# Optimization experiments

Hardware: AMD Instinct MI355X
Metric: run time of the kernel (lower is better)

## Reference

```python
import jax, jax.numpy as jnp
import numpy as np

N, S, E, H = 4, 2048, 1024, 16
D = E // H  # head dim = 64


def setup_inputs() -> dict:
    key = jax.random.key(0)
    ks = jax.random.split(key, 8)
    return {
        "values": jax.random.normal(ks[0], (N, S, E), dtype=jnp.float32),
        "keys": jax.random.normal(ks[1], (N, S, E), dtype=jnp.float32),
        "queries": jax.random.normal(ks[2], (N, S, E), dtype=jnp.float32),
        "mask": jnp.ones((N, 1, 1, S), dtype=jnp.int32),
        "Wv": jax.random.normal(ks[3], (D, D), dtype=jnp.float32) / np.sqrt(D),
        "Wk": jax.random.normal(ks[4], (D, D), dtype=jnp.float32) / np.sqrt(D),
        "Wq": jax.random.normal(ks[5], (D, D), dtype=jnp.float32) / np.sqrt(D),
        "W_out": jax.random.normal(ks[6], (E, E), dtype=jnp.float32) / np.sqrt(E),
        "b_out": jnp.zeros((E,), dtype=jnp.float32),
    }


def reference(values, keys, queries, mask, Wv, Wk, Wq, W_out, b_out):
    n, q_len = queries.shape[0], queries.shape[1]
    v = values.reshape(n, -1, H, D)
    k = keys.reshape(n, -1, H, D)
    q = queries.reshape(n, q_len, H, D)
    # per-head linear projections (torch Linear: x @ W.T), shared across heads
    v = jnp.einsum('nlhd,ed->nlhe', v, Wv)
    k = jnp.einsum('nlhd,ed->nlhe', k, Wk)
    q = jnp.einsum('nqhd,ed->nqhe', q, Wq)
    # full score tensor [n, h, q, k], faithful to the original einsum
    energy = jnp.einsum('nqhd,nkhd->nhqk', q, k)
    energy = jnp.where(mask == 0, jnp.float32(-1e20), energy)
    # NOTE: original scales by sqrt(embed_size), not sqrt(head_dim)
    attention = jax.nn.softmax(energy / jnp.sqrt(jnp.float32(E)), axis=3)
    out = jnp.einsum('nhql,nlhd->nqhd', attention, v).reshape(n, q_len, E)
    out = out @ W_out.T + b_out
    return out
```

## Files before the change

kernel.cpp:

```cpp
#include <hip/hip_runtime.h>
#include <stdint.h>

#define N_B 4
#define SEQ 2048
#define EMB 1024
#define NH  16
#define HD  64
#define NHT 64
#define BQ  128
#define BK  64

typedef __attribute__((ext_vector_type(8))) short bf16x8;
typedef __attribute__((ext_vector_type(4))) short bf16x4;
typedef __attribute__((ext_vector_type(4))) float f32x4;

__device__ __forceinline__ short f2bf(float x) {
  unsigned u = __float_as_uint(x);
  u += 0x7fffu + ((u >> 16) & 1u);
  return (short)(u >> 16);
}

__device__ __forceinline__ void glds16(const short* g, short* l) {
  __builtin_amdgcn_global_load_lds(
      (const __attribute__((address_space(1))) unsigned int*)g,
      (__attribute__((address_space(3))) unsigned int*)l, 16, 0, 0);
}

__device__ __forceinline__ int swz_src(int lane) {
  return (((lane & 7) ^ ((lane >> 3) & 7)) * 8) + ((lane >> 3) * 64);
}
__device__ __forceinline__ int swz_rd(int r, int k) {
  return r * 64 + ((k ^ (r & 7)) * 8);
}

__global__ __launch_bounds__(256) void cvt_kernel(const float* __restrict__ W,
                                                  short* __restrict__ Wb) {
  int idx = (blockIdx.x * 256 + threadIdx.x) * 4;
  f32x4 v = *(const f32x4*)(W + idx);
  bf16x4 p;
  p.x = f2bf(v.x); p.y = f2bf(v.y); p.z = f2bf(v.z); p.w = f2bf(v.w);
  *(bf16x4*)(Wb + idx) = p;
}

__global__ __launch_bounds__(256) void projm_kernel(const float* __restrict__ X,
                                                    const float* __restrict__ W,
                                                    short* __restrict__ out,
                                                    int transposed) {
  __shared__ __attribute__((aligned(16))) short Xs[128 * 64];
  __shared__ __attribute__((aligned(16))) short Ws[64 * 64];
  int tid = threadIdx.x;
  int w = tid >> 6, lane = tid & 63;
  int quad = lane >> 4, l15 = lane & 15;
  int sb = blockIdx.x * 128;
  int nh = blockIdx.y;
  int n = nh >> 4, h = nh & 15;
  int r4 = tid >> 2, c0 = (tid & 3) * 16;
  int ch0 = c0 >> 3;
#pragma unroll
  for (int rr = 0; rr < 2; rr++) {
    int row = rr * 64 + r4;
    const float* gp = X + ((size_t)(n * SEQ + sb + row)) * EMB + h * HD + c0;
    f32x4 a = *(const f32x4*)gp, b = *(const f32x4*)(gp + 4);
    f32x4 c = *(const f32x4*)(gp + 8), d = *(const f32x4*)(gp + 12);
    bf16x8 p0, p1;
    p0[0]=f2bf(a.x); p0[1]=f2bf(a.y); p0[2]=f2bf(a.z); p0[3]=f2bf(a.w);
    p0[4]=f2bf(b.x); p0[5]=f2bf(b.y); p0[6]=f2bf(b.z); p0[7]=f2bf(b.w);
    p1[0]=f2bf(c.x); p1[1]=f2bf(c.y); p1[2]=f2bf(c.z); p1[3]=f2bf(c.w);
    p1[4]=f2bf(d.x); p1[5]=f2bf(d.y); p1[6]=f2bf(d.z); p1[7]=f2bf(d.w);
    *(bf16x8*)&Xs[row * 64 + ((ch0 ^ (row & 7)) * 8)] = p0;
    *(bf16x8*)&Xs[row * 64 + (((ch0 + 1) ^ (row & 7)) * 8)] = p1;
  }
  {
    int e = r4;
    const float* wp = W + e * HD + c0;
    f32x4 a = *(const f32x4*)wp, b = *(const f32x4*)(wp + 4);
    f32x4 c = *(const f32x4*)(wp + 8), d = *(const f32x4*)(wp + 12);
    bf16x8 p0, p1;
    p0[0]=f2bf(a.x); p0[1]=f2bf(a.y); p0[2]=f2bf(a.z); p0[3]=f2bf(a.w);
    p0[4]=f2bf(b.x); p0[5]=f2bf(b.y); p0[6]=f2bf(b.z); p0[7]=f2bf(b.w);
    p1[0]=f2bf(c.x); p1[1]=f2bf(c.y); p1[2]=f2bf(c.z); p1[3]=f2bf(c.w);
    p1[4]=f2bf(d.x); p1[5]=f2bf(d.y); p1[6]=f2bf(d.z); p1[7]=f2bf(d.w);
    *(bf16x8*)&Ws[e * 64 + ((ch0 ^ (e & 7)) * 8)] = p0;
    *(bf16x8*)&Ws[e * 64 + (((ch0 + 1) ^ (e & 7)) * 8)] = p1;
  }
  __syncthreads();
  f32x4 acc[2][4] = {};
#pragma unroll
  for (int ch = 0; ch < 2; ch++) {
    bf16x8 af[2], bfr[4];
#pragma unroll
    for (int mi = 0; mi < 2; mi++)
      af[mi] = *(const bf16x8*)&Xs[swz_rd(w * 32 + mi * 16 + l15, ch * 4 + quad)];
#pragma unroll
    for (int ni = 0; ni < 4; ni++)
      bfr[ni] = *(const bf16x8*)&Ws[swz_rd(ni * 16 + l15, ch * 4 + quad)];
#pragma unroll
    for (int mi = 0; mi < 2; mi++)
#pragma unroll
      for (int ni = 0; ni < 4; ni++)
        acc[mi][ni] = __builtin_amdgcn_mfma_f32_16x16x32_bf16(af[mi], bfr[ni], acc[mi][ni], 0, 0, 0);
  }
  if (!transposed) {
#pragma unroll
    for (int mi = 0; mi < 2; mi++)
#pragma unroll
      for (int ni = 0; ni < 4; ni++)
#pragma unroll
        for (int r = 0; r < 4; r++) {
          int s = sb + w * 32 + mi * 16 + quad * 4 + r;
          out[((size_t)nh * SEQ + s) * HD + ni * 16 + l15] = f2bf(acc[mi][ni][r]);
        }
  } else {
#pragma unroll
    for (int mi = 0; mi < 2; mi++)
#pragma unroll
      for (int ni = 0; ni < 4; ni++) {
        int e2 = ni * 16 + l15;
        int s0 = sb + w * 32 + mi * 16 + quad * 4;
        bf16x4 pk;
        pk.x = f2bf(acc[mi][ni][0]); pk.y = f2bf(acc[mi][ni][1]);
        pk.z = f2bf(acc[mi][ni][2]); pk.w = f2bf(acc[mi][ni][3]);
        *(bf16x4*)(out + ((size_t)nh * HD + e2) * SEQ + s0) = pk;
      }
  }
}

__global__ __launch_bounds__(256, 3) void attn_kernel(
    const short* __restrict__ Qp, const short* __restrict__ Kp,
    const short* __restrict__ Vp, const int* __restrict__ maskp,
    short* __restrict__ AO) {
  __shared__ __attribute__((aligned(16))) short Ks[64 * 64];
  __shared__ __attribute__((aligned(16))) short Vts[64 * 64];
  __shared__ __attribute__((aligned(16))) short Qs[128 * 64];
  __shared__ __attribute__((aligned(16))) short Ps[4][32 * 72];
  __shared__ int maskS[64];

  int tid = threadIdx.x;
  int w = tid >> 6, lane = tid & 63;
  int quad = lane >> 4, l15 = lane & 15;
  int nh = blockIdx.x;
  int qt0 = blockIdx.y * BQ;
  int n = nh >> 4, h = nh & 15;
  const float csc = 0.04508422f;
  int ssrc = swz_src(lane);

  const short* qbase = Qp + ((size_t)nh * SEQ + qt0) * HD;
#pragma unroll
  for (int i = 0; i < 4; i++) {
    int idx = (w * 4 + i) * 512;
    glds16(qbase + idx + ssrc, &Qs[idx]);
  }
  __syncthreads();
  bf16x8 qf[2][2];
#pragma unroll
  for (int nt = 0; nt < 2; nt++)
#pragma unroll
    for (int ch = 0; ch < 2; ch++)
      qf[nt][ch] = *(const bf16x8*)&Qs[swz_rd(w * 32 + nt * 16 + l15, ch * 4 + quad)];

  f32x4 Oacc[2][4] = {};
  float lsum[2] = {0.f, 0.f};

  for (int kt = 0; kt < SEQ / BK; kt++) {
    int k0 = kt * BK;
    __syncthreads();
    const short* kb = Kp + ((size_t)nh * SEQ + k0) * HD;
#pragma unroll
    for (int i = 0; i < 2; i++) {
      int idx = (w * 2 + i) * 512;
      glds16(kb + idx + ssrc, &Ks[idx]);
    }
#pragma unroll
    for (int i = 0; i < 2; i++) {
      int ii = w * 2 + i;
      int d = ii * 8 + (lane >> 3);
      const short* vb = Vp + ((size_t)nh * HD + d) * SEQ + k0 +
                        (((lane & 7) ^ ((lane >> 3) & 7)) * 8);
      glds16(vb, &Vts[ii * 512]);
    }
    if (tid < 64) maskS[tid] = maskp[n * SEQ + k0 + tid];
    __syncthreads();

    unsigned long long mb = __ballot(maskS[lane] != 0);

    f32x4 st[4][2];
#pragma unroll
    for (int mt = 0; mt < 4; mt++) {
      bf16x8 kf0 = *(const bf16x8*)&Ks[swz_rd(mt * 16 + l15, quad)];
      bf16x8 kf1 = *(const bf16x8*)&Ks[swz_rd(mt * 16 + l15, 4 + quad)];
#pragma unroll
      for (int nt = 0; nt < 2; nt++) {
        f32x4 a = {0.f, 0.f, 0.f, 0.f};
        a = __builtin_amdgcn_mfma_f32_16x16x32_bf16(kf0, qf[nt][0], a, 0, 0, 0);
        a = __builtin_amdgcn_mfma_f32_16x16x32_bf16(kf1, qf[nt][1], a, 0, 0, 0);
        st[mt][nt] = a;
      }
    }
    if (mb != ~0ull) {
#pragma unroll
      for (int mt = 0; mt < 4; mt++)
#pragma unroll
        for (int r = 0; r < 4; r++) {
          int kk = mt * 16 + quad * 4 + r;
          if (!((mb >> kk) & 1)) { st[mt][0][r] = -1e20f; st[mt][1][r] = -1e20f; }
        }
    }
#pragma unroll
    for (int nt = 0; nt < 2; nt++)
#pragma unroll
      for (int mt = 0; mt < 4; mt++)
#pragma unroll
        for (int r = 0; r < 4; r++) {
          float p = __builtin_amdgcn_exp2f(st[mt][nt][r] * csc);
          st[mt][nt][r] = p;
          lsum[nt] += p;
        }
    short* psw = &Ps[w][0];
#pragma unroll
    for (int nt = 0; nt < 2; nt++)
#pragma unroll
      for (int mt = 0; mt < 4; mt++) {
        bf16x4 pk;
        pk.x = f2bf(st[mt][nt][0]); pk.y = f2bf(st[mt][nt][1]);
        pk.z = f2bf(st[mt][nt][2]); pk.w = f2bf(st[mt][nt][3]);
        *(bf16x4*)&psw[(nt * 16 + l15) * 72 + mt * 16 + quad * 4] = pk;
      }
    __builtin_amdgcn_wave_barrier();

#pragma unroll
    for (int ch = 0; ch < 2; ch++) {
      bf16x8 pf[2];
#pragma unroll
      for (int qt = 0; qt < 2; qt++)
        pf[qt] = *(const bf16x8*)&psw[(qt * 16 + l15) * 72 + ch * 32 + quad * 8];
#pragma unroll
      for (int dt = 0; dt < 4; dt++) {
        bf16x8 vf = *(const bf16x8*)&Vts[swz_rd(dt * 16 + l15, ch * 4 + quad)];
#pragma unroll
        for (int qt = 0; qt < 2; qt++)
          Oacc[qt][dt] = __builtin_amdgcn_mfma_f32_16x16x32_bf16(pf[qt], vf, Oacc[qt][dt], 0, 0, 0);
      }
    }
  }
#pragma unroll
  for (int nt = 0; nt < 2; nt++) {
    lsum[nt] += __shfl_xor(lsum[nt], 16);
    lsum[nt] += __shfl_xor(lsum[nt], 32);
  }
#pragma unroll
  for (int qt = 0; qt < 2; qt++)
#pragma unroll
    for (int r = 0; r < 4; r++) {
      float lr = __shfl(lsum[qt], quad * 4 + r);
      float inv = 1.0f / lr;
      int qrow = qt0 + w * 32 + qt * 16 + quad * 4 + r;
      size_t rowb = ((size_t)n * SEQ + qrow) * EMB + h * HD;
#pragma unroll
      for (int dt = 0; dt < 4; dt++)
        AO[rowb + dt * 16 + l15] = f2bf(Oacc[qt][dt][r] * inv);
    }
}

__global__ __launch_bounds__(256, 3) void gemm_kernel(const short* __restrict__ A,
                                                      const short* __restrict__ B,
                                                      const float* __restrict__ bias,
                                                      float* __restrict__ C) {
  __shared__ __attribute__((aligned(16))) short As[128 * 64];
  __shared__ __attribute__((aligned(16))) short Bs[128 * 64];
  int tid = threadIdx.x;
  int w = tid >> 6, lane = tid & 63;
  int quad = lane >> 4, l15 = lane & 15;
  int m0 = blockIdx.x * 128, n0 = blockIdx.y * 128;
  int mw = (w & 1) * 64, nw = (w >> 1) * 64;
  int lrow = lane >> 3;
  int lcg = ((lane & 7) ^ ((lane >> 3) & 7)) * 8;
  f32x4 acc[4][4] = {};
  for (int kt = 0; kt < 16; kt++) {
    int k0 = kt * 64;
    __syncthreads();
#pragma unroll
    for (int i = 0; i < 4; i++) {
      int ii = w * 4 + i;
      int r = ii * 8 + lrow;
      glds16(A + (size_t)(m0 + r) * 1024 + k0 + lcg, &As[ii * 512]);
      glds16(B + (size_t)(n0 + r) * 1024 + k0 + lcg, &Bs[ii * 512]);
    }
    __syncthreads();
#pragma unroll
    for (int ch = 0; ch < 2; ch++) {
      bf16x8 af[4], bfr[4];
#pragma unroll
      for (int mi = 0; mi < 4; mi++)
        af[mi] = *(const bf16x8*)&As[swz_rd(mw + mi * 16 + l15, ch * 4 + quad)];
#pragma unroll
      for (int ni = 0; ni < 4; ni++)
        bfr[ni] = *(const bf16x8*)&Bs[swz_rd(nw + ni * 16 + l15, ch * 4 + quad)];
#pragma unroll
      for (int mi = 0; mi < 4; mi++)
#pragma unroll
        for (int ni = 0; ni < 4; ni++)
          acc[mi][ni] = __builtin_amdgcn_mfma_f32_16x16x32_bf16(af[mi], bfr[ni], acc[mi][ni], 0, 0, 0);
    }
  }
#pragma unroll
  for (int ni = 0; ni < 4; ni++) {
    int col = n0 + nw + ni * 16 + l15;
    float bv = bias[col];
#pragma unroll
    for (int mi = 0; mi < 4; mi++) {
      int rb = m0 + mw + mi * 16 + quad * 4;
#pragma unroll
      for (int r = 0; r < 4; r++)
        C[(size_t)(rb + r) * 1024 + col] = acc[mi][ni][r] + bv;
    }
  }
}

extern "C" void kernel_launch(void* const* d_in, const int* in_sizes, int n_in,
                              void* d_out, int out_size, void* d_ws, size_t ws_size,
                              hipStream_t stream) {
  const float* values  = (const float*)d_in[0];
  const float* keys    = (const float*)d_in[1];
  const float* queries = (const float*)d_in[2];
  const int*   mask    = (const int*)d_in[3];
  const float* Wv = (const float*)d_in[4];
  const float* Wk = (const float*)d_in[5];
  const float* Wq = (const float*)d_in[6];
  const float* Wo = (const float*)d_in[7];
  const float* bo = (const float*)d_in[8];
  float* out = (float*)d_out;

  short* ws = (short*)d_ws;
  short* Qp = ws;
  short* Kp = Qp + (size_t)NHT * SEQ * HD;
  short* Vp = Kp + (size_t)NHT * SEQ * HD;
  short* AO = Vp + (size_t)NHT * SEQ * HD;
  short* Wb = AO + (size_t)N_B * SEQ * EMB;

  cvt_kernel<<<dim3(1024), dim3(256), 0, stream>>>(Wo, Wb);
  dim3 pg(SEQ / 128, NHT);
  projm_kernel<<<pg, dim3(256), 0, stream>>>(queries, Wq, Qp, 0);
  projm_kernel<<<pg, dim3(256), 0, stream>>>(keys, Wk, Kp, 0);
  projm_kernel<<<pg, dim3(256), 0, stream>>>(values, Wv, Vp, 1);
  dim3 ag(NHT, SEQ / BQ);
  attn_kernel<<<ag, dim3(256), 0, stream>>>(Qp, Kp, Vp, mask, AO);
  dim3 gg(8192 / 128, 1024 / 128);
  gemm_kernel<<<gg, dim3(256), 0, stream>>>(AO, Wb, bo, out);
}
```

Baseline: 303.9 us.

## Double-buffer attention and GEMM loads, merge projection launches, use packed bf16 converts

Folds the weight-conversion kernel and the three projection launches into one launch, using grid z to pick Q, K, V or the W_out conversion. The attention kernel now double-buffers K/V/mask tiles in LDS so the next tile's load overlaps current compute, with one barrier per iteration. Its P scratch reuses the Q buffer with an XOR swizzle instead of padding, which lowers LDS use. The output GEMM is double-buffered too, with launch bounds lowered to 2 blocks per CU because it now needs twice the LDS. Float-to-bf16 rounding uses the hardware packed-convert builtin when it is available.

```diff
diff --git a/kernel.cpp b/kernel.cpp
--- a/kernel.cpp
+++ b/kernel.cpp
@@ -20,6 +20,18 @@
   return (short)(u >> 16);
 }
 
+#if __has_builtin(__builtin_amdgcn_cvt_pk_bf16_f32)
+typedef __attribute__((ext_vector_type(2))) __bf16 bf16v2;
+__device__ __forceinline__ unsigned pkbf(float a, float b) {
+  bf16v2 r = __builtin_amdgcn_cvt_pk_bf16_f32(a, b);
+  union { bf16v2 v; unsigned u; } c; c.v = r; return c.u;
+}
+#else
+__device__ __forceinline__ unsigned pkbf(float a, float b) {
+  return (unsigned)(unsigned short)f2bf(a) | ((unsigned)(unsigned short)f2bf(b) << 16);
+}
+#endif
+
 __device__ __forceinline__ void glds16(const short* g, short* l) {
   __builtin_amdgcn_global_load_lds(
       (const __attribute__((address_space(1))) unsigned int*)g,
@@ -33,22 +45,28 @@
   return r * 64 + ((k ^ (r & 7)) * 8);
 }
 
-__global__ __launch_bounds__(256) void cvt_kernel(const float* __restrict__ W,
-                                                  short* __restrict__ Wb) {
-  int idx = (blockIdx.x * 256 + threadIdx.x) * 4;
-  f32x4 v = *(const f32x4*)(W + idx);
-  bf16x4 p;
-  p.x = f2bf(v.x); p.y = f2bf(v.y); p.z = f2bf(v.z); p.w = f2bf(v.w);
-  *(bf16x4*)(Wb + idx) = p;
-}
-
-__global__ __launch_bounds__(256) void projm_kernel(const float* __restrict__ X,
-                                                    const float* __restrict__ W,
-                                                    short* __restrict__ out,
-                                                    int transposed) {
+__global__ __launch_bounds__(256) void projm_kernel(
+    const float* __restrict__ Xq, const float* __restrict__ Xk, const float* __restrict__ Xv,
+    const float* __restrict__ Wq, const float* __restrict__ Wk, const float* __restrict__ Wv,
+    short* __restrict__ Qp, short* __restrict__ Kp, short* __restrict__ Vp,
+    const float* __restrict__ Wo, short* __restrict__ Wb) {
+  int tid = threadIdx.x;
+  int z = blockIdx.z;
+  if (z == 3) {
+    int flat = blockIdx.x + blockIdx.y * 16;
+    int idx = (flat * 256 + tid) * 4;
+    f32x4 v = *(const f32x4*)(Wo + idx);
+    uint2 u; u.x = pkbf(v.x, v.y); u.y = pkbf(v.z, v.w);
+    *(uint2*)(Wb + idx) = u;
+    return;
+  }
+  const float* X = (z == 0) ? Xq : (z == 1) ? Xk : Xv;
+  const float* W = (z == 0) ? Wq : (z == 1) ? Wk : Wv;
+  short* out = (z == 0) ? Qp : (z == 1) ? Kp : Vp;
+  int transposed = (z == 2);
+
   __shared__ __attribute__((aligned(16))) short Xs[128 * 64];
   __shared__ __attribute__((aligned(16))) short Ws[64 * 64];
-  int tid = threadIdx.x;
   int w = tid >> 6, lane = tid & 63;
   int quad = lane >> 4, l15 = lane & 15;
   int sb = blockIdx.x * 128;
@@ -62,26 +80,26 @@
     const float* gp = X + ((size_t)(n * SEQ + sb + row)) * EMB + h * HD + c0;
     f32x4 a = *(const f32x4*)gp, b = *(const f32x4*)(gp + 4);
     f32x4 c = *(const f32x4*)(gp + 8), d = *(const f32x4*)(gp + 12);
-    bf16x8 p0, p1;
-    p0[0]=f2bf(a.x); p0[1]=f2bf(a.y); p0[2]=f2bf(a.z); p0[3]=f2bf(a.w);
-    p0[4]=f2bf(b.x); p0[5]=f2bf(b.y); p0[6]=f2bf(b.z); p0[7]=f2bf(b.w);
-    p1[0]=f2bf(c.x); p1[1]=f2bf(c.y); p1[2]=f2bf(c.z); p1[3]=f2bf(c.w);
-    p1[4]=f2bf(d.x); p1[5]=f2bf(d.y); p1[6]=f2bf(d.z); p1[7]=f2bf(d.w);
-    *(bf16x8*)&Xs[row * 64 + ((ch0 ^ (row & 7)) * 8)] = p0;
-    *(bf16x8*)&Xs[row * 64 + (((ch0 + 1) ^ (row & 7)) * 8)] = p1;
+    uint4 u0, u1;
+    u0.x = pkbf(a.x, a.y); u0.y = pkbf(a.z, a.w);
+    u0.z = pkbf(b.x, b.y); u0.w = pkbf(b.z, b.w);
+    u1.x = pkbf(c.x, c.y); u1.y = pkbf(c.z, c.w);
+    u1.z = pkbf(d.x, d.y); u1.w = pkbf(d.z, d.w);
+    *(uint4*)&Xs[row * 64 + ((ch0 ^ (row & 7)) * 8)] = u0;
+    *(uint4*)&Xs[row * 64 + (((ch0 + 1) ^ (row & 7)) * 8)] = u1;
   }
   {
     int e = r4;
     const float* wp = W + e * HD + c0;
     f32x4 a = *(const f32x4*)wp, b = *(const f32x4*)(wp + 4);
     f32x4 c = *(const f32x4*)(wp + 8), d = *(const f32x4*)(wp + 12);
-    bf16x8 p0, p1;
-    p0[0]=f2bf(a.x); p0[1]=f2bf(a.y); p0[2]=f2bf(a.z); p0[3]=f2bf(a.w);
-    p0[4]=f2bf(b.x); p0[5]=f2bf(b.y); p0[6]=f2bf(b.z); p0[7]=f2bf(b.w);
-    p1[0]=f2bf(c.x); p1[1]=f2bf(c.y); p1[2]=f2bf(c.z); p1[3]=f2bf(c.w);
-    p1[4]=f2bf(d.x); p1[5]=f2bf(d.y); p1[6]=f2bf(d.z); p1[7]=f2bf(d.w);
-    *(bf16x8*)&Ws[e * 64 + ((ch0 ^ (e & 7)) * 8)] = p0;
-    *(bf16x8*)&Ws[e * 64 + (((ch0 + 1) ^ (e & 7)) * 8)] = p1;
+    uint4 u0, u1;
+    u0.x = pkbf(a.x, a.y); u0.y = pkbf(a.z, a.w);
+    u0.z = pkbf(b.x, b.y); u0.w = pkbf(b.z, b.w);
+    u1.x = pkbf(c.x, c.y); u1.y = pkbf(c.z, c.w);
+    u1.z = pkbf(d.x, d.y); u1.w = pkbf(d.z, d.w);
+    *(uint4*)&Ws[e * 64 + ((ch0 ^ (e & 7)) * 8)] = u0;
+    *(uint4*)&Ws[e * 64 + (((ch0 + 1) ^ (e & 7)) * 8)] = u1;
   }
   __syncthreads();
   f32x4 acc[2][4] = {};
@@ -117,23 +135,21 @@
       for (int ni = 0; ni < 4; ni++) {
         int e2 = ni * 16 + l15;
         int s0 = sb + w * 32 + mi * 16 + quad * 4;
-        bf16x4 pk;
-        pk.x = f2bf(acc[mi][ni][0]); pk.y = f2bf(acc[mi][ni][1]);
-        pk.z = f2bf(acc[mi][ni][2]); pk.w = f2bf(acc[mi][ni][3]);
-        *(bf16x4*)(out + ((size_t)nh * HD + e2) * SEQ + s0) = pk;
+        uint2 u;
+        u.x = pkbf(acc[mi][ni][0], acc[mi][ni][1]);
+        u.y = pkbf(acc[mi][ni][2], acc[mi][ni][3]);
+        *(uint2*)(out + ((size_t)nh * HD + e2) * SEQ + s0) = u;
       }
   }
 }
 
 __global__ __launch_bounds__(256, 3) void attn_kernel(
-    const short* __restrict__ Qp, const short* __restrict__ Kp,
-    const short* __restrict__ Vp, const int* __restrict__ maskp,
+    const short* __restrict__ Qg, const short* __restrict__ Kg,
+    const short* __restrict__ Vg, const int* __restrict__ maskp,
     short* __restrict__ AO) {
-  __shared__ __attribute__((aligned(16))) short Ks[64 * 64];
-  __shared__ __attribute__((aligned(16))) short Vts[64 * 64];
-  __shared__ __attribute__((aligned(16))) short Qs[128 * 64];
-  __shared__ __attribute__((aligned(16))) short Ps[4][32 * 72];
-  __shared__ int maskS[64];
+  __shared__ __attribute__((aligned(16))) short KV[2][2][64 * 64];
+  __shared__ __attribute__((aligned(16))) short QP[128 * 64];
+  __shared__ int maskS[2][64];
 
   int tid = threadIdx.x;
   int w = tid >> 6, lane = tid & 63;
@@ -143,51 +159,64 @@
   int n = nh >> 4, h = nh & 15;
   const float csc = 0.04508422f;
   int ssrc = swz_src(lane);
-
-  const short* qbase = Qp + ((size_t)nh * SEQ + qt0) * HD;
+  int vrow = lane >> 3;
+  int vcg = (((lane & 7) ^ ((lane >> 3) & 7)) * 8);
+
+  const short* kb = Kg + (size_t)nh * SEQ * HD;
+  const short* vb = Vg + (size_t)nh * HD * SEQ;
+
+  const short* qbase = Qg + ((size_t)nh * SEQ + qt0) * HD;
 #pragma unroll
   for (int i = 0; i < 4; i++) {
     int idx = (w * 4 + i) * 512;
-    glds16(qbase + idx + ssrc, &Qs[idx]);
-  }
+    glds16(qbase + idx + ssrc, &QP[idx]);
+  }
+#pragma unroll
+  for (int i = 0; i < 2; i++) {
+    int idx = (w * 2 + i) * 512;
+    glds16(kb + idx + ssrc, &KV[0][0][idx]);
+    int d = (w * 2 + i) * 8 + vrow;
+    glds16(vb + (size_t)d * SEQ + vcg, &KV[0][1][idx]);
+  }
+  if (tid < 64) maskS[0][tid] = maskp[n * SEQ + tid];
   __syncthreads();
+
   bf16x8 qf[2][2];
 #pragma unroll
   for (int nt = 0; nt < 2; nt++)
 #pragma unroll
     for (int ch = 0; ch < 2; ch++)
-      qf[nt][ch] = *(const bf16x8*)&Qs[swz_rd(w * 32 + nt * 16 + l15, ch * 4 + quad)];
+      qf[nt][ch] = *(const bf16x8*)&QP[swz_rd(w * 32 + nt * 16 + l15, ch * 4 + quad)];
 
   f32x4 Oacc[2][4] = {};
   float lsum[2] = {0.f, 0.f};
+  short* psw = &QP[w * 2048];
 
   for (int kt = 0; kt < SEQ / BK; kt++) {
-    int k0 = kt * BK;
-    __syncthreads();
-    const short* kb = Kp + ((size_t)nh * SEQ + k0) * HD;
-#pragma unroll
-    for (int i = 0; i < 2; i++) {
-      int idx = (w * 2 + i) * 512;
-      glds16(kb + idx + ssrc, &Ks[idx]);
-    }
-#pragma unroll
-    for (int i = 0; i < 2; i++) {
-      int ii = w * 2 + i;
-      int d = ii * 8 + (lane >> 3);
-      const short* vb = Vp + ((size_t)nh * HD + d) * SEQ + k0 +
-                        (((lane & 7) ^ ((lane >> 3) & 7)) * 8);
-      glds16(vb, &Vts[ii * 512]);
-    }
-    if (tid < 64) maskS[tid] = maskp[n * SEQ + k0 + tid];
-    __syncthreads();
-
-    unsigned long long mb = __ballot(maskS[lane] != 0);
+    int cur = kt & 1;
+    const short* Kc = KV[cur][0];
+    const short* Vc = KV[cur][1];
+    if (kt + 1 < SEQ / BK) {
+      int k0n = (kt + 1) * BK;
+      short* Kn = KV[cur ^ 1][0];
+      short* Vn = KV[cur ^ 1][1];
+#pragma unroll
+      for (int i = 0; i < 2; i++) {
+        int idx = (w * 2 + i) * 512;
+        glds16(kb + (size_t)k0n * HD + idx + ssrc, Kn + idx);
+        int d = (w * 2 + i) * 8 + vrow;
+        glds16(vb + (size_t)d * SEQ + k0n + vcg, Vn + idx);
+      }
+      if (tid < 64) maskS[cur ^ 1][tid] = maskp[n * SEQ + k0n + tid];
+    }
+
+    unsigned long long mb = __ballot(maskS[cur][lane] != 0);
 
     f32x4 st[4][2];
 #pragma unroll
     for (int mt = 0; mt < 4; mt++) {
-      bf16x8 kf0 = *(const bf16x8*)&Ks[swz_rd(mt * 16 + l15, quad)];
-      bf16x8 kf1 = *(const bf16x8*)&Ks[swz_rd(mt * 16 + l15, 4 + quad)];
+      bf16x8 kf0 = *(const bf16x8*)&Kc[swz_rd(mt * 16 + l15, quad)];
+      bf16x8 kf1 = *(const bf16x8*)&Kc[swz_rd(mt * 16 + l15, 4 + quad)];
 #pragma unroll
       for (int nt = 0; nt < 2; nt++) {
         f32x4 a = {0.f, 0.f, 0.f, 0.f};
@@ -215,16 +244,17 @@
           st[mt][nt][r] = p;
           lsum[nt] += p;
         }
-    short* psw = &Ps[w][0];
-#pragma unroll
-    for (int nt = 0; nt < 2; nt++)
+#pragma unroll
+    for (int nt = 0; nt < 2; nt++) {
+      int wrow = nt * 16 + l15;
 #pragma unroll
       for (int mt = 0; mt < 4; mt++) {
-        bf16x4 pk;
-        pk.x = f2bf(st[mt][nt][0]); pk.y = f2bf(st[mt][nt][1]);
-        pk.z = f2bf(st[mt][nt][2]); pk.w = f2bf(st[mt][nt][3]);
-        *(bf16x4*)&psw[(nt * 16 + l15) * 72 + mt * 16 + quad * 4] = pk;
-      }
+        uint2 u;
+        u.x = pkbf(st[mt][nt][0], st[mt][nt][1]);
+        u.y = pkbf(st[mt][nt][2], st[mt][nt][3]);
+        *(uint2*)&psw[wrow * 64 + (((mt * 2 + (quad >> 1)) ^ (wrow & 7)) * 8) + (quad & 1) * 4] = u;
+      }
+    }
     __builtin_amdgcn_wave_barrier();
 
 #pragma unroll
@@ -232,15 +262,16 @@
       bf16x8 pf[2];
 #pragma unroll
       for (int qt = 0; qt < 2; qt++)
-        pf[qt] = *(const bf16x8*)&psw[(qt * 16 + l15) * 72 + ch * 32 + quad * 8];
+        pf[qt] = *(const bf16x8*)&psw[swz_rd(qt * 16 + l15, ch * 4 + quad)];
 #pragma unroll
       for (int dt = 0; dt < 4; dt++) {
-        bf16x8 vf = *(const bf16x8*)&Vts[swz_rd(dt * 16 + l15, ch * 4 + quad)];
+        bf16x8 vf = *(const bf16x8*)&Vc[swz_rd(dt * 16 + l15, ch * 4 + quad)];
 #pragma unroll
         for (int qt = 0; qt < 2; qt++)
           Oacc[qt][dt] = __builtin_amdgcn_mfma_f32_16x16x32_bf16(pf[qt], vf, Oacc[qt][dt], 0, 0, 0);
       }
     }
+    __syncthreads();
   }
 #pragma unroll
   for (int nt = 0; nt < 2; nt++) {
@@ -261,12 +292,12 @@
     }
 }
 
-__global__ __launch_bounds__(256, 3) void gemm_kernel(const short* __restrict__ A,
+__global__ __launch_bounds__(256, 2) void gemm_kernel(const short* __restrict__ A,
                                                       const short* __restrict__ B,
                                                       const float* __restrict__ bias,
                                                       float* __restrict__ C) {
-  __shared__ __attribute__((aligned(16))) short As[128 * 64];
-  __shared__ __attribute__((aligned(16))) short Bs[128 * 64];
+  __shared__ __attribute__((aligned(16))) short As[2][128 * 64];
+  __shared__ __attribute__((aligned(16))) short Bs[2][128 * 64];
   int tid = threadIdx.x;
   int w = tid >> 6, lane = tid & 63;
   int quad = lane >> 4, l15 = lane & 15;
@@ -275,32 +306,42 @@
   int lrow = lane >> 3;
   int lcg = ((lane & 7) ^ ((lane >> 3) & 7)) * 8;
   f32x4 acc[4][4] = {};
+#pragma unroll
+  for (int i = 0; i < 4; i++) {
+    int ii = w * 4 + i;
+    int r = ii * 8 + lrow;
+    glds16(A + (size_t)(m0 + r) * 1024 + lcg, &As[0][ii * 512]);
+    glds16(B + (size_t)(n0 + r) * 1024 + lcg, &Bs[0][ii * 512]);
+  }
+  __syncthreads();
   for (int kt = 0; kt < 16; kt++) {
-    int k0 = kt * 64;
-    __syncthreads();
-#pragma unroll
-    for (int i = 0; i < 4; i++) {
-      int ii = w * 4 + i;
-      int r = ii * 8 + lrow;
-      glds16(A + (size_t)(m0 + r) * 1024 + k0 + lcg, &As[ii * 512]);
-      glds16(B + (size_t)(n0 + r) * 1024 + k0 + lcg, &Bs[ii * 512]);
-    }
-    __syncthreads();
+    int cur = kt & 1;
+    if (kt < 15) {
+      int k0n = (kt + 1) * 64;
+#pragma unroll
+      for (int i = 0; i < 4; i++) {
+        int ii = w * 4 + i;
+        int r = ii * 8 + lrow;
+        glds16(A + (size_t)(m0 + r) * 1024 + k0n + lcg, &As[cur ^ 1][ii * 512]);
+        glds16(B + (size_t)(n0 + r) * 1024 + k0n + lcg, &Bs[cur ^ 1][ii * 512]);
+      }
+    }
 #pragma unroll
     for (int ch = 0; ch < 2; ch++) {
       bf16x8 af[4], bfr[4];
 #pragma unroll
       for (int mi = 0; mi < 4; mi++)
-        af[mi] = *(const bf16x8*)&As[swz_rd(mw + mi * 16 + l15, ch * 4 + quad)];
+        af[mi] = *(const bf16x8*)&As[cur][swz_rd(mw + mi * 16 + l15, ch * 4 + quad)];
 #pragma unroll
       for (int ni = 0; ni < 4; ni++)
-        bfr[ni] = *(const bf16x8*)&Bs[swz_rd(nw + ni * 16 + l15, ch * 4 + quad)];
+        bfr[ni] = *(const bf16x8*)&Bs[cur][swz_rd(nw + ni * 16 + l15, ch * 4 + quad)];
 #pragma unroll
       for (int mi = 0; mi < 4; mi++)
 #pragma unroll
         for (int ni = 0; ni < 4; ni++)
           acc[mi][ni] = __builtin_amdgcn_mfma_f32_16x16x32_bf16(af[mi], bfr[ni], acc[mi][ni], 0, 0, 0);
     }
+    __syncthreads();
   }
 #pragma unroll
   for (int ni = 0; ni < 4; ni++) {
@@ -337,11 +378,9 @@
   short* AO = Vp + (size_t)NHT * SEQ * HD;
   short* Wb = AO + (size_t)N_B * SEQ * EMB;
 
-  cvt_kernel<<<dim3(1024), dim3(256), 0, stream>>>(Wo, Wb);
-  dim3 pg(SEQ / 128, NHT);
-  projm_kernel<<<pg, dim3(256), 0, stream>>>(queries, Wq, Qp, 0);
-  projm_kernel<<<pg, dim3(256), 0, stream>>>(keys, Wk, Kp, 0);
-  projm_kernel<<<pg, dim3(256), 0, stream>>>(values, Wv, Vp, 1);
+  dim3 pg(SEQ / 128, NHT, 4);
+  projm_kernel<<<pg, dim3(256), 0, stream>>>(queries, keys, values, Wq, Wk, Wv,
+                                             Qp, Kp, Vp, Wo, Wb);
   dim3 ag(NHT, SEQ / BQ);
   attn_kernel<<<ag, dim3(256), 0, stream>>>(Qp, Kp, Vp, mask, AO);
   dim3 gg(8192 / 128, 1024 / 128);
```

Result: faster. 285.9 us (-5.9%).
